# Kernel tuning notes

Measured on AMD Instinct MI355X. Metric: run time of the kernel, lower is better.

Reference implementation:

```python
import math
import jax, jax.numpy as jnp
import numpy as np


def setup_inputs() -> dict:
    key = jax.random.key(0)
    k1, k2 = jax.random.split(key)
    x = jax.random.normal(k1, (32, 3, 64, 64), dtype=jnp.float32)   # (B,C,H,W)
    y = jax.random.normal(k2, (512, 3, 64, 64), dtype=jnp.float32)  # (N,C,H,W)
    return {"x": x, "y": y}


def reference(x, y):
    # Faithful to torch rfft/irfft with normalized=True (unitary / 'ortho' scaling).
    B, C, H, W = x.shape
    scale = math.sqrt(H * W)  # self.N in the torch module
    X = jnp.fft.rfft2(x, norm="ortho")  # (B,C,H,W//2+1) complex
    Y = jnp.fft.rfft2(y, norm="ortho")  # (N,C,H,W//2+1) complex
    # conj(X) . Y summed over channels, fused as one complex contraction
    G = jnp.einsum("bchw,nchw->bnhw", jnp.conj(X), Y)  # (B,N,H,W//2+1)
    g = jnp.fft.irfft2(G, s=(H, W), norm="ortho") * scale  # (B,N,H,W)
    m = jnp.max(g, axis=(-2, -1))  # MaxPool2d(kernel=input_size) -> (B,N)
    xx = jnp.linalg.norm(x.reshape(B, -1), axis=-1)[:, None]  # (B,1)
    yy = jnp.linalg.norm(y.reshape(y.shape[0], -1), axis=-1)[None, :]  # (1,N)
    return m / xx / yy
```

## Files before the change

kernel.cpp:

```cpp
#include <hip/hip_runtime.h>
#include <math.h>

#define FBINS 2112
#define CSC 66

typedef float cplx __attribute__((ext_vector_type(2)));
typedef __fp16 half2v __attribute__((ext_vector_type(2)));
#define MK2(a,b) (cplx){(float)(a), (float)(b)}

__device__ __forceinline__ cplx shufxy(cplx a){ return __builtin_shufflevector(a, a, 1, 0); }
template<int S> __device__ __forceinline__ cplx imul(cplx a){
    return (S > 0) ? shufxy(a) * MK2(-1.f, 1.f) : shufxy(a) * MK2(1.f, -1.f);
}
template<int S> __device__ __forceinline__ cplx cmul_tw(cplx a, cplx w){
    cplx ws = shufxy(w);
    return (S > 0) ? a.x*w + a.y*(ws*MK2(-1.f, 1.f))
                   : a.x*(w*MK2(1.f, -1.f)) + a.y*ws;
}

__device__ __forceinline__ unsigned pack16(float a, float b){
    half2v h = __builtin_amdgcn_cvt_pkrtz(a, b);
    return __builtin_bit_cast(unsigned, h);
}
__device__ __forceinline__ half2v h2(unsigned u){ return __builtin_bit_cast(half2v, u); }
__device__ __forceinline__ float fdot2(half2v a, half2v b, float c){
#if __has_builtin(__builtin_amdgcn_fdot2)
    return __builtin_amdgcn_fdot2(a, b, c, false);
#else
    return c + (float)a.x*(float)b.x + (float)a.y*(float)b.y;
#endif
}
__device__ __forceinline__ void dotw(unsigned ux, unsigned uy, float& r, float& s){
    unsigned ys = ((uy >> 16) | (uy << 16)) ^ 0x80000000u;
    r = fdot2(h2(ux), h2(uy), r);
    s = fdot2(h2(ux), h2(ys), s);
}
__device__ __forceinline__ void dotw_i(unsigned ux, unsigned uy, cplx& v){
    float rr = 0.f, ss = 0.f;
    dotw(ux, uy, rr, ss);
    v += MK2(-ss, rr);
}

__device__ __constant__ float TWC[112] = {
  1.f,0.f, 1.f,0.f, 1.f,0.f, 1.f,0.f, 1.f,0.f, 1.f,0.f, 1.f,0.f,
  0.9951847267f,0.0980171403f, 0.9807852804f,0.1950903220f, 0.9569403357f,0.2902846773f,
  0.9238795325f,0.3826834324f, 0.8819212643f,0.4713967368f, 0.8314696123f,0.5555702330f,
  0.7730104534f,0.6343932842f,
  0.9807852804f,0.1950903220f, 0.9238795325f,0.3826834324f, 0.8314696123f,0.5555702330f,
  0.7071067812f,0.7071067812f, 0.5555702330f,0.8314696123f, 0.3826834324f,0.9238795325f,
  0.1950903220f,0.9807852804f,
  0.9569403357f,0.2902846773f, 0.8314696123f,0.5555702330f, 0.6343932842f,0.7730104534f,
  0.3826834324f,0.9238795325f, 0.0980171403f,0.9951847267f, -0.1950903220f,0.9807852804f,
  -0.4713967368f,0.8819212643f,
  0.9238795325f,0.3826834324f, 0.7071067812f,0.7071067812f, 0.3826834324f,0.9238795325f,
  0.f,1.f, -0.3826834324f,0.9238795325f, -0.7071067812f,0.7071067812f,
  -0.9238795325f,0.3826834324f,
  0.8819212643f,0.4713967368f, 0.5555702330f,0.8314696123f, 0.0980171403f,0.9951847267f,
  -0.3826834324f,0.9238795325f, -0.7730104534f,0.6343932842f, -0.9807852804f,0.1950903220f,
  -0.9569403357f,-0.2902846773f,
  0.8314696123f,0.5555702330f, 0.3826834324f,0.9238795325f, -0.1950903220f,0.9807852804f,
  -0.7071067812f,0.7071067812f, -0.9807852804f,0.1950903220f, -0.9238795325f,-0.3826834324f,
  -0.5555702330f,-0.8314696123f,
  0.7730104534f,0.6343932842f, 0.1950903220f,0.9807852804f, -0.4713967368f,0.8819212643f,
  -0.9238795325f,0.3826834324f, -0.9569403357f,-0.2902846773f, -0.5555702330f,-0.8314696123f,
  0.0980171403f,-0.9951847267f
};
__device__ __forceinline__ void load_tw(int j, cplx wj[7]){
    #pragma unroll
    for (int k=0;k<7;++k) wj[k] = MK2(TWC[(j*7+k)*2], TWC[(j*7+k)*2+1]);
}

template<int S>
__device__ __forceinline__ void dft8(cplx v[8]) {
    const float C = 0.70710678118654752440f;
    cplx t0=v[0]+v[4], t4=v[0]-v[4];
    cplx t1=v[1]+v[5], t5=v[1]-v[5];
    cplx t2=v[2]+v[6], t6=v[2]-v[6];
    cplx t3=v[3]+v[7], t7=v[3]-v[7];
    cplx u0=t0+t2, u2=t0-t2;
    cplx u1=t1+t3, u3=t1-t3;
    v[0]=u0+u1; v[4]=u0-u1;
    cplx m3=imul<S>(u3);
    v[2]=u2+m3; v[6]=u2-m3;
    cplx z0=t4;
    cplx z1 = C*(t5 + imul<S>(t5));
    cplx z2 = imul<S>(t6);
    cplx z3 = C*(imul<S>(t7) - t7);
    cplx w0=z0+z2, w2=z0-z2;
    cplx w1=z1+z3, w3=z1-z3;
    v[1]=w0+w1; v[5]=w0-w1;
    cplx mb=imul<S>(w3);
    v[3]=w2+mb; v[7]=w2-mb;
}

template<int S>
__device__ __forceinline__ void fft64_from_regs(
    cplx v[8], cplx* __restrict__ mem, const int wa[8], const int ra[8],
    const cplx wj[7])
{
    dft8<S>(v);
    #pragma unroll
    for (int k=1;k<8;++k) v[k] = cmul_tw<S>(v[k], wj[k-1]);
    #pragma unroll
    for (int k=0;k<8;++k) mem[wa[k]] = v[k];
    #pragma unroll
    for (int n=0;n<8;++n) v[n] = mem[ra[n]];
    dft8<S>(v);
}

__global__ __launch_bounds__(256) void fwd_fft_kernel(
    const float* __restrict__ x, const float* __restrict__ y,
    unsigned* __restrict__ Xh, unsigned* __restrict__ Yh,
    float* __restrict__ pn)
{
    __shared__ __align__(16) cplx CL[2176];
    __shared__ float red[4];
    const int tid = threadIdx.x, G = tid>>3, j = tid&7;
    const int blk = blockIdx.x;
    const bool isX = blk < 96;

    cplx wj[7]; load_tw(j, wj);
    int wa[8], ra[8];
    {
        int base = CSC*G;
        #pragma unroll
        for (int k=0;k<8;++k) wa[k] = base + 8*j + (k^j);
        #pragma unroll
        for (int k=0;k<8;++k) ra[k] = base + 8*k + (j^k);
    }

    const float* img = (isX ? x + (size_t)blk * 4096
                            : y + (size_t)(blk - 96) * 4096);
    unsigned* o = (isX ? Xh + (size_t)blk * FBINS
                       : Yh + (size_t)(blk - 96) * FBINS);

    {
        cplx v[8];
        float ns = 0.f;
        #pragma unroll
        for (int nn=0;nn<8;++nn){ int w=8*nn+j;
            float a = img[64*G + w], c = img[64*(G+32) + w];
            v[nn] = MK2(a, c);
            ns = fmaf(a, a, ns); ns = fmaf(c, c, ns); }
        #pragma unroll
        for (int off = 32; off; off >>= 1) ns += __shfl_xor(ns, off);
        if ((tid & 63) == 0) red[tid >> 6] = ns;
        fft64_from_regs<-1>(v, CL, wa, ra, wj);
        int base = CSC*G;
        #pragma unroll
        for (int k=0;k<8;++k) CL[base + j + 8*k] = v[k];
    }
    __syncthreads();

    {
        cplx v[8];
        if (G == 0) {
            #pragma unroll
            for (int nn=0;nn<8;++nn){
                int r=8*nn+j, p=r&31, hi=r>>5;
                cplx a0  = CL[CSC*p + 0];
                cplx a32 = CL[CSC*p + 32];
                v[nn] = hi ? MK2(a0.y, a32.y) : MK2(a0.x, a32.x);
            }
        } else {
            const int c = G;
            #pragma unroll
            for (int nn=0;nn<8;++nn){
                int r=8*nn+j, p=r&31, hi=r>>5;
                cplx A  = CL[CSC*p + c];
                cplx Bm = CL[CSC*p + 64 - c];
                if (!hi) v[nn] = 0.5f*(A + Bm*MK2(1.f,-1.f));
                else     v[nn] = 0.5f*(shufxy(A)*MK2(1.f,-1.f) + shufxy(Bm));
            }
        }
        __syncthreads();
        fft64_from_regs<-1>(v, CL, wa, ra, wj);
        int base = CSC*G;
        #pragma unroll
        for (int k=0;k<8;++k) CL[base + j + 8*k] = v[k];
    }
    __syncthreads();

    for (int i = tid; i < FBINS; i += 256) {
        int wp = i>>6, h = i&63;
        cplx r;
        if (wp == 0) {
            int h2i = (64-h)&63;
            cplx av = CL[h], bb = CL[h2i];
            r = 0.5f*(av + bb*MK2(1.f,-1.f));
        } else if (wp == 32) {
            int h2i = (64-h)&63;
            cplx av = CL[h], bb = CL[h2i];
            r = 0.5f*(shufxy(av)*MK2(1.f,-1.f) + shufxy(bb));
        } else {
            r = CL[CSC*wp + h];
        }
        int slot = (wp << 6) | ((h & 7) << 3) | (h >> 3);
        o[slot] = pack16(r.x, r.y);
    }
    if (tid == 0) pn[blk] = red[0] + red[1] + red[2] + red[3];
}

__global__ __launch_bounds__(256) void corr_kernel(
    const unsigned* __restrict__ Xh, const unsigned* __restrict__ Yh,
    const float* __restrict__ px, const float* __restrict__ py,
    float* __restrict__ out)
{
    __shared__ __align__(16) cplx CL[2176];
    __shared__ float red[4];
    const int tid = threadIdx.x, G = tid>>3, j = tid&7;

    const int blk = blockIdx.x;
    const int xcd = blk & 7, idx = blk >> 3;
    const int n = xcd*64 + (idx & 63);
    const int b = idx >> 6;

    const float x2 = px[3*b] + px[3*b+1] + px[3*b+2];
    const float y2 = py[3*n] + py[3*n+1] + py[3*n+2];
    const float dinv = rsqrtf(x2 * y2) * (1.0f/4096.0f);

    int wa[8], ra[8];
    {
        int base = CSC*G;
        #pragma unroll
        for (int k=0;k<8;++k) wa[k] = base + 8*j + (k^j);
        #pragma unroll
        for (int k=0;k<8;++k) ra[k] = base + 8*k + (j^k);
    }

    const uint4* pX4 = (const uint4*)Xh + (size_t)b * 3 * 528;
    const uint4* pY4 = (const uint4*)Yh + (size_t)n * 3 * 528;
    cplx v[8];
    {
        float r[8], s[8];
        #pragma unroll
        for (int k=0;k<8;++k){ r[k]=0.f; s[k]=0.f; }
        const int off = 16*G + 2*j;
        #pragma unroll
        for (int ch = 0; ch < 3; ++ch) {
            uint4 x0 = pX4[ch*528 + off], x1 = pX4[ch*528 + off + 1];
            uint4 y0 = pY4[ch*528 + off], y1 = pY4[ch*528 + off + 1];
            dotw(x0.x, y0.x, r[0], s[0]);  dotw(x0.y, y0.y, r[1], s[1]);
            dotw(x0.z, y0.z, r[2], s[2]);  dotw(x0.w, y0.w, r[3], s[3]);
            dotw(x1.x, y1.x, r[4], s[4]);  dotw(x1.y, y1.y, r[5], s[5]);
            dotw(x1.z, y1.z, r[6], s[6]);  dotw(x1.w, y1.w, r[7], s[7]);
        }
        #pragma unroll
        for (int k=0;k<8;++k) v[k] = MK2(r[k], s[k]);
    }
    if (G == 0) {
        const int off = 512 + 2*j;
        #pragma unroll
        for (int ch = 0; ch < 3; ++ch) {
            uint4 x0 = pX4[ch*528 + off], x1 = pX4[ch*528 + off + 1];
            uint4 y0 = pY4[ch*528 + off], y1 = pY4[ch*528 + off + 1];
            dotw_i(x0.x, y0.x, v[0]);  dotw_i(x0.y, y0.y, v[1]);
            dotw_i(x0.z, y0.z, v[2]);  dotw_i(x0.w, y0.w, v[3]);
            dotw_i(x1.x, y1.x, v[4]);  dotw_i(x1.y, y1.y, v[5]);
            dotw_i(x1.z, y1.z, v[6]);  dotw_i(x1.w, y1.w, v[7]);
        }
    }

    cplx wj[7]; load_tw(j, wj);

    fft64_from_regs<1>(v, CL, wa, ra, wj);
    #pragma unroll
    for (int k=0;k<4;++k)
        *(float4*)&CL[CSC*G + 2*(j+8*k)] =
            make_float4(v[k].x, v[k].y, v[k+4].x, v[k+4].y);
    __syncthreads();

    float m = -3.4e38f;
    {
        if (j == 0) {
            float4 f = *(float4*)&CL[2*G];
            v[0] = MK2(f.x, f.z);
            v[4] = MK2(f.y, f.w);
        } else {
            float4 f = *(float4*)&CL[CSC*j + 2*G];
            v[0] = MK2(f.x,f.y) + imul<1>(MK2(f.z,f.w));
            float4 g2 = *(float4*)&CL[CSC*(32-j) + 2*G];
            v[4] = MK2(g2.x,g2.y)*MK2(1.f,-1.f) + shufxy(MK2(g2.z,g2.w));
        }
        #pragma unroll
        for (int nn=1;nn<4;++nn){
            int w = 8*nn + j;
            float4 f = *(float4*)&CL[CSC*w + 2*G];
            v[nn] = MK2(f.x,f.y) + imul<1>(MK2(f.z,f.w));
        }
        #pragma unroll
        for (int nn=5;nn<8;++nn){
            int w2 = 64 - (8*nn + j);
            float4 f = *(float4*)&CL[CSC*w2 + 2*G];
            v[nn] = MK2(f.x,f.y)*MK2(1.f,-1.f) + shufxy(MK2(f.z,f.w));
        }
        __syncthreads();
        fft64_from_regs<1>(v, CL, wa, ra, wj);
        #pragma unroll
        for (int k=0;k<8;++k) m = fmaxf(m, fmaxf(v[k].x, v[k].y));
    }
    #pragma unroll
    for (int off = 32; off; off >>= 1) m = fmaxf(m, __shfl_xor(m, off));
    if ((tid & 63) == 0) red[tid >> 6] = m;
    __syncthreads();
    if (tid == 0) {
        float mm = fmaxf(fmaxf(red[0], red[1]), fmaxf(red[2], red[3]));
        out[b*512 + n] = mm * dinv;
    }
}

extern "C" void kernel_launch(void* const* d_in, const int* in_sizes, int n_in,
                              void* d_out, int out_size, void* d_ws, size_t ws_size,
                              hipStream_t stream) {
    const float* x = (const float*)d_in[0];
    const float* y = (const float*)d_in[1];
    float* out = (float*)d_out;

    unsigned* Xh = (unsigned*)d_ws;
    unsigned* Yh = Xh + 96 * FBINS;
    float* pn = (float*)(Yh + 1536 * FBINS);
    float* px = pn;
    float* py = pn + 96;

    fwd_fft_kernel<<<1632, 256, 0, stream>>>(x, y, Xh, Yh, pn);
    corr_kernel<<<16384, 256, 0, stream>>>(Xh, Yh, px, py, out);
}
```

Baseline: 79.31 us.

## Process four batch items per block, reusing Y spectrum registers

```diff
diff --git a/kernel.cpp b/kernel.cpp
--- a/kernel.cpp
+++ b/kernel.cpp
@@ -3,6 +3,7 @@
 
 #define FBINS 2112
 #define CSC 66
+#define NPB 4
 
 typedef float cplx __attribute__((ext_vector_type(2)));
 typedef __fp16 half2v __attribute__((ext_vector_type(2)));
@@ -31,9 +32,9 @@
 #endif
 }
 __device__ __forceinline__ void dotw(unsigned ux, unsigned uy, float& r, float& s){
-    unsigned ys = ((uy >> 16) | (uy << 16)) ^ 0x80000000u;
+    unsigned xs = ((ux >> 16) | (ux << 16)) ^ 0x00008000u;
     r = fdot2(h2(ux), h2(uy), r);
-    s = fdot2(h2(ux), h2(ys), s);
+    s = fdot2(h2(xs), h2(uy), s);
 }
 __device__ __forceinline__ void dotw_i(unsigned ux, unsigned uy, cplx& v){
     float rr = 0.f, ss = 0.f;
@@ -201,7 +202,7 @@
     if (tid == 0) pn[blk] = red[0] + red[1] + red[2] + red[3];
 }
 
-__global__ __launch_bounds__(256) void corr_kernel(
+__global__ __launch_bounds__(256, 8) void corr_kernel(
     const unsigned* __restrict__ Xh, const unsigned* __restrict__ Yh,
     const float* __restrict__ px, const float* __restrict__ py,
     float* __restrict__ out)
@@ -212,100 +213,112 @@
 
     const int blk = blockIdx.x;
     const int xcd = blk & 7, idx = blk >> 3;
-    const int n = xcd*64 + (idx & 63);
-    const int b = idx >> 6;
-
-    const float x2 = px[3*b] + px[3*b+1] + px[3*b+2];
+    const int n  = xcd*64 + (idx & 63);
+    const int bg = idx >> 6;
+
+    int wa[8], ra[8];
+    {
+        int base = CSC*G;
+        #pragma unroll
+        for (int k=0;k<8;++k) wa[k] = base + 8*j + (k^j);
+        #pragma unroll
+        for (int k=0;k<8;++k) ra[k] = base + 8*k + (j^k);
+    }
+    cplx wj[7]; load_tw(j, wj);
+
     const float y2 = py[3*n] + py[3*n+1] + py[3*n+2];
-    const float dinv = rsqrtf(x2 * y2) * (1.0f/4096.0f);
-
-    int wa[8], ra[8];
-    {
-        int base = CSC*G;
-        #pragma unroll
-        for (int k=0;k<8;++k) wa[k] = base + 8*j + (k^j);
-        #pragma unroll
-        for (int k=0;k<8;++k) ra[k] = base + 8*k + (j^k);
-    }
-
-    const uint4* pX4 = (const uint4*)Xh + (size_t)b * 3 * 528;
+
     const uint4* pY4 = (const uint4*)Yh + (size_t)n * 3 * 528;
-    cplx v[8];
-    {
-        float r[8], s[8];
-        #pragma unroll
-        for (int k=0;k<8;++k){ r[k]=0.f; s[k]=0.f; }
+    uint4 yv[3][2];
+    {
         const int off = 16*G + 2*j;
         #pragma unroll
-        for (int ch = 0; ch < 3; ++ch) {
-            uint4 x0 = pX4[ch*528 + off], x1 = pX4[ch*528 + off + 1];
-            uint4 y0 = pY4[ch*528 + off], y1 = pY4[ch*528 + off + 1];
-            dotw(x0.x, y0.x, r[0], s[0]);  dotw(x0.y, y0.y, r[1], s[1]);
-            dotw(x0.z, y0.z, r[2], s[2]);  dotw(x0.w, y0.w, r[3], s[3]);
-            dotw(x1.x, y1.x, r[4], s[4]);  dotw(x1.y, y1.y, r[5], s[5]);
-            dotw(x1.z, y1.z, r[6], s[6]);  dotw(x1.w, y1.w, r[7], s[7]);
-        }
-        #pragma unroll
-        for (int k=0;k<8;++k) v[k] = MK2(r[k], s[k]);
-    }
-    if (G == 0) {
-        const int off = 512 + 2*j;
-        #pragma unroll
-        for (int ch = 0; ch < 3; ++ch) {
-            uint4 x0 = pX4[ch*528 + off], x1 = pX4[ch*528 + off + 1];
-            uint4 y0 = pY4[ch*528 + off], y1 = pY4[ch*528 + off + 1];
-            dotw_i(x0.x, y0.x, v[0]);  dotw_i(x0.y, y0.y, v[1]);
-            dotw_i(x0.z, y0.z, v[2]);  dotw_i(x0.w, y0.w, v[3]);
-            dotw_i(x1.x, y1.x, v[4]);  dotw_i(x1.y, y1.y, v[5]);
-            dotw_i(x1.z, y1.z, v[6]);  dotw_i(x1.w, y1.w, v[7]);
-        }
-    }
-
-    cplx wj[7]; load_tw(j, wj);
-
-    fft64_from_regs<1>(v, CL, wa, ra, wj);
-    #pragma unroll
-    for (int k=0;k<4;++k)
-        *(float4*)&CL[CSC*G + 2*(j+8*k)] =
-            make_float4(v[k].x, v[k].y, v[k+4].x, v[k+4].y);
-    __syncthreads();
-
-    float m = -3.4e38f;
-    {
-        if (j == 0) {
-            float4 f = *(float4*)&CL[2*G];
-            v[0] = MK2(f.x, f.z);
-            v[4] = MK2(f.y, f.w);
-        } else {
-            float4 f = *(float4*)&CL[CSC*j + 2*G];
-            v[0] = MK2(f.x,f.y) + imul<1>(MK2(f.z,f.w));
-            float4 g2 = *(float4*)&CL[CSC*(32-j) + 2*G];
-            v[4] = MK2(g2.x,g2.y)*MK2(1.f,-1.f) + shufxy(MK2(g2.z,g2.w));
-        }
-        #pragma unroll
-        for (int nn=1;nn<4;++nn){
-            int w = 8*nn + j;
-            float4 f = *(float4*)&CL[CSC*w + 2*G];
-            v[nn] = MK2(f.x,f.y) + imul<1>(MK2(f.z,f.w));
-        }
-        #pragma unroll
-        for (int nn=5;nn<8;++nn){
-            int w2 = 64 - (8*nn + j);
-            float4 f = *(float4*)&CL[CSC*w2 + 2*G];
-            v[nn] = MK2(f.x,f.y)*MK2(1.f,-1.f) + shufxy(MK2(f.z,f.w));
-        }
+        for (int ch=0; ch<3; ++ch){
+            yv[ch][0] = pY4[ch*528 + off];
+            yv[ch][1] = pY4[ch*528 + off + 1];
+        }
+    }
+
+    for (int q = 0; q < NPB; ++q) {
+        const int b = bg*NPB + q;
+        const uint4* pX4 = (const uint4*)Xh + (size_t)b * 3 * 528;
+
+        cplx v[8];
+        {
+            float r[8], s[8];
+            #pragma unroll
+            for (int k=0;k<8;++k){ r[k]=0.f; s[k]=0.f; }
+            const int off = 16*G + 2*j;
+            #pragma unroll
+            for (int ch = 0; ch < 3; ++ch) {
+                uint4 x0 = pX4[ch*528 + off], x1 = pX4[ch*528 + off + 1];
+                dotw(x0.x, yv[ch][0].x, r[0], s[0]);  dotw(x0.y, yv[ch][0].y, r[1], s[1]);
+                dotw(x0.z, yv[ch][0].z, r[2], s[2]);  dotw(x0.w, yv[ch][0].w, r[3], s[3]);
+                dotw(x1.x, yv[ch][1].x, r[4], s[4]);  dotw(x1.y, yv[ch][1].y, r[5], s[5]);
+                dotw(x1.z, yv[ch][1].z, r[6], s[6]);  dotw(x1.w, yv[ch][1].w, r[7], s[7]);
+            }
+            #pragma unroll
+            for (int k=0;k<8;++k) v[k] = MK2(r[k], s[k]);
+        }
+        if (G == 0) {
+            const int off = 512 + 2*j;
+            #pragma unroll
+            for (int ch = 0; ch < 3; ++ch) {
+                uint4 x0 = pX4[ch*528 + off], x1 = pX4[ch*528 + off + 1];
+                uint4 y0 = pY4[ch*528 + off], y1 = pY4[ch*528 + off + 1];
+                dotw_i(x0.x, y0.x, v[0]);  dotw_i(x0.y, y0.y, v[1]);
+                dotw_i(x0.z, y0.z, v[2]);  dotw_i(x0.w, y0.w, v[3]);
+                dotw_i(x1.x, y1.x, v[4]);  dotw_i(x1.y, y1.y, v[5]);
+                dotw_i(x1.z, y1.z, v[6]);  dotw_i(x1.w, y1.w, v[7]);
+            }
+        }
+
+        fft64_from_regs<1>(v, CL, wa, ra, wj);
+        #pragma unroll
+        for (int k=0;k<4;++k)
+            *(float4*)&CL[CSC*G + 2*(j+8*k)] =
+                make_float4(v[k].x, v[k].y, v[k+4].x, v[k+4].y);
         __syncthreads();
-        fft64_from_regs<1>(v, CL, wa, ra, wj);
-        #pragma unroll
-        for (int k=0;k<8;++k) m = fmaxf(m, fmaxf(v[k].x, v[k].y));
-    }
-    #pragma unroll
-    for (int off = 32; off; off >>= 1) m = fmaxf(m, __shfl_xor(m, off));
-    if ((tid & 63) == 0) red[tid >> 6] = m;
-    __syncthreads();
-    if (tid == 0) {
-        float mm = fmaxf(fmaxf(red[0], red[1]), fmaxf(red[2], red[3]));
-        out[b*512 + n] = mm * dinv;
+
+        float m = -3.4e38f;
+        {
+            if (j == 0) {
+                float4 f = *(float4*)&CL[2*G];
+                v[0] = MK2(f.x, f.z);
+                v[4] = MK2(f.y, f.w);
+            } else {
+                float4 f = *(float4*)&CL[CSC*j + 2*G];
+                v[0] = MK2(f.x,f.y) + imul<1>(MK2(f.z,f.w));
+                float4 g2 = *(float4*)&CL[CSC*(32-j) + 2*G];
+                v[4] = MK2(g2.x,g2.y)*MK2(1.f,-1.f) + shufxy(MK2(g2.z,g2.w));
+            }
+            #pragma unroll
+            for (int nn=1;nn<4;++nn){
+                int w = 8*nn + j;
+                float4 f = *(float4*)&CL[CSC*w + 2*G];
+                v[nn] = MK2(f.x,f.y) + imul<1>(MK2(f.z,f.w));
+            }
+            #pragma unroll
+            for (int nn=5;nn<8;++nn){
+                int w2 = 64 - (8*nn + j);
+                float4 f = *(float4*)&CL[CSC*w2 + 2*G];
+                v[nn] = MK2(f.x,f.y)*MK2(1.f,-1.f) + shufxy(MK2(f.z,f.w));
+            }
+            __syncthreads();
+            fft64_from_regs<1>(v, CL, wa, ra, wj);
+            #pragma unroll
+            for (int k=0;k<8;++k) m = fmaxf(m, fmaxf(v[k].x, v[k].y));
+        }
+        #pragma unroll
+        for (int off = 32; off; off >>= 1) m = fmaxf(m, __shfl_xor(m, off));
+        if ((tid & 63) == 0) red[tid >> 6] = m;
+        __syncthreads();
+        if (tid == 0) {
+            const float x2 = px[3*b] + px[3*b+1] + px[3*b+2];
+            const float dinv = rsqrtf(x2 * y2) * (1.0f/4096.0f);
+            float mm = fmaxf(fmaxf(red[0], red[1]), fmaxf(red[2], red[3]));
+            out[b*512 + n] = mm * dinv;
+        }
     }
 }
 
@@ -323,5 +336,5 @@
     float* py = pn + 96;
 
     fwd_fft_kernel<<<1632, 256, 0, stream>>>(x, y, Xh, Yh, pn);
-    corr_kernel<<<16384, 256, 0, stream>>>(Xh, Yh, px, py, out);
-}
+    corr_kernel<<<32/NPB*512, 256, 0, stream>>>(Xh, Yh, px, py, out);
+}
```

Result: slower. 274.3 us (+245.9%).
